# Performance work log

Measured on AMD Instinct MI355X. Metric: run time of the kernel, lower is better.

Reference implementation:

```python
import jax, jax.numpy as jnp
import numpy as np

N = 2048  # number of graph nodes


def setup_inputs() -> dict:
    key = jax.random.key(0)
    k1, k2, k3, k4 = jax.random.split(key, 4)
    # dense non-negative adjacency / association matrix
    A = jax.random.uniform(k1, (N, N), dtype=jnp.float32)
    # GTConv weights: layer0.conv1, layer0.conv2, layer1.conv1 (each (2,1,1,1))
    w1a = jax.random.normal(k2, (2, 1, 1, 1), dtype=jnp.float32)
    w1b = jax.random.normal(k3, (2, 1, 1, 1), dtype=jnp.float32)
    w2a = jax.random.normal(k4, (2, 1, 1, 1), dtype=jnp.float32)
    return {"A": A, "w1a": w1a, "w1b": w1b, "w2a": w2a}


def _gtconv(A4, w):
    # A4: (1,1,n,n); w: (2,1,1,1). softmax over dim=1 (singleton -> ones),
    # broadcast-multiply -> (2,1,n,n), sum over dim 0 -> (1,n,n)
    sw = jax.nn.softmax(w, axis=1)
    return jnp.sum(A4 * sw, axis=0)


def _norm(H):
    # H: (n,n). H <- diag(deg)^-1 @ (H + I), expressed as a row-scale
    # (identical math to the diagonal mm in the original).
    n = H.shape[0]
    H = H + jnp.eye(n, dtype=H.dtype)
    deg = jnp.sum(H, axis=1)
    deg = jnp.where(deg <= 1e-10, jnp.ones_like(deg), deg)
    return H / deg[:, None]


def reference(A, w1a, w1b, w2a):
    A4 = A[None, None]  # (1,1,n,n) after the forward's unsqueeze + broadcast
    # layer 0 (first=True)
    a = _gtconv(A4, w1a)            # (1,n,n)
    b = _gtconv(A4, w1b)            # (1,n,n)
    H = jnp.matmul(a, b)            # (1,n,n)
    # layer 1 (first=False): normalization of H[0], then bmm with conv(A)
    H_ = _norm(H[0])[None]          # (1,n,n)
    a2 = _gtconv(A4, w2a)           # (1,n,n)
    H2 = jnp.matmul(H_, a2)         # (1,n,n)
    return H2
```

## Files before the change

kernel.cpp:

```cpp
#include <hip/hip_runtime.h>
#include <stdint.h>

#define N 2048
#define TILE 128
#define BK 32
#define KI (N / BK)
#define LDSW 40
#define NN ((size_t)N * (size_t)N)

typedef unsigned short u16;
typedef __bf16 bf16x8 __attribute__((ext_vector_type(8)));
typedef unsigned short ushortx8 __attribute__((ext_vector_type(8)));
typedef float floatx4 __attribute__((ext_vector_type(4)));

static __device__ __forceinline__ u16 f2bf(float f) {
  unsigned int u = __builtin_bit_cast(unsigned int, f);
  return (u16)((u + 0x7fffu + ((u >> 16) & 1u)) >> 16);
}
static __device__ __forceinline__ float bf2f(u16 h) {
  unsigned int u = ((unsigned int)h) << 16;
  return __builtin_bit_cast(float, u);
}

__global__ void cast_tr(const float* __restrict__ A, u16* __restrict__ Ab,
                        u16* __restrict__ Abt) {
  __shared__ float tile[32][33];
  const int tx = threadIdx.x, ty = threadIdx.y;
  const int c = blockIdx.x * 32 + tx;
#pragma unroll
  for (int i = 0; i < 4; i++) {
    const int r = blockIdx.y * 32 + ty + i * 8;
    const float v = A[r * N + c];
    Ab[r * N + c] = f2bf(v);
    tile[ty + i * 8][tx] = v;
  }
  __syncthreads();
  const int r2 = blockIdx.y * 32 + tx;
#pragma unroll
  for (int i = 0; i < 4; i++) {
    const int c2 = blockIdx.x * 32 + ty + i * 8;
    Abt[c2 * N + r2] = f2bf(tile[tx][ty + i * 8]);
  }
}

__device__ __forceinline__ void gemm_core(const u16* __restrict__ L,
                                          const u16* __restrict__ Rt,
                                          floatx4 acc[4][2]) {
  __shared__ __align__(16) u16 As[2][TILE * LDSW];
  __shared__ __align__(16) u16 Bs[2][TILE * LDSW];

  const int t = threadIdx.x;
  const int row0 = blockIdx.y * TILE;
  const int col0 = blockIdx.x * TILE;

  const int srow = t >> 2;
  const int sc = (t & 3) * 8;
  const u16* gA = L + (size_t)(row0 + srow) * N + sc;
  const u16* gB = Rt + (size_t)(col0 + srow) * N + sc;
  const int woff = srow * LDSW + sc;

  const int lane = t & 63;
  const int w = t >> 6;
  const int wr = (w >> 2) * 64;
  const int wc = (w & 3) * 32;
  const int lr = lane & 15;
  const int q = lane >> 4;
  const int aoff = (wr + lr) * LDSW + q * 8;
  const int boff = (wc + lr) * LDSW + q * 8;

#pragma unroll
  for (int i = 0; i < 4; i++)
#pragma unroll
    for (int j = 0; j < 2; j++) acc[i][j] = (floatx4){0.f, 0.f, 0.f, 0.f};

  ushortx8 rA[4], rB[4];
#pragma unroll
  for (int s = 0; s < 3; s++) {
    rA[s] = *(const ushortx8*)(gA + s * BK);
    rB[s] = *(const ushortx8*)(gB + s * BK);
  }
  *(ushortx8*)(&As[0][woff]) = rA[0];
  *(ushortx8*)(&Bs[0][woff]) = rB[0];
  __syncthreads();

#define GSTEP(i, s, cur, nxt)                                                \
  {                                                                          \
    if ((i) + 3 < KI) {                                                      \
      rA[((s) + 3) & 3] = *(const ushortx8*)(gA + ((i) + 3) * BK);           \
      rB[((s) + 3) & 3] = *(const ushortx8*)(gB + ((i) + 3) * BK);           \
    }                                                                        \
    bf16x8 af[4], bfr[2];                                                    \
    _Pragma("unroll") for (int mt = 0; mt < 4; mt++) af[mt] =                \
        __builtin_bit_cast(bf16x8,                                           \
                           *(const ushortx8*)&As[cur][aoff + mt * 16 * LDSW]); \
    _Pragma("unroll") for (int nt = 0; nt < 2; nt++) bfr[nt] =               \
        __builtin_bit_cast(bf16x8,                                           \
                           *(const ushortx8*)&Bs[cur][boff + nt * 16 * LDSW]); \
    _Pragma("unroll") for (int mt = 0; mt < 4; mt++)                         \
        _Pragma("unroll") for (int nt = 0; nt < 2; nt++) acc[mt][nt] =       \
            __builtin_amdgcn_mfma_f32_16x16x32_bf16(af[mt], bfr[nt],         \
                                                    acc[mt][nt], 0, 0, 0);   \
    __syncthreads();   \
    if ((i) + 1 < KI) {                                                      \
      *(ushortx8*)(&As[nxt][woff]) = rA[((s) + 1) & 3];                      \
      *(ushortx8*)(&Bs[nxt][woff]) = rB[((s) + 1) & 3];                      \
    }                                                                        \
    __syncthreads();                      \
  }

  for (int io = 0; io < KI; io += 4) {
    GSTEP(io + 0, 0, 0, 1)
    GSTEP(io + 1, 1, 1, 0)
    GSTEP(io + 2, 2, 0, 1)
    GSTEP(io + 3, 3, 1, 0)
  }
#undef GSTEP
}

__global__ __launch_bounds__(512, 2) void gemm_aa(const u16* __restrict__ Ab,
                                                  const u16* __restrict__ Abt,
                                                  u16* __restrict__ Mb) {
  floatx4 acc[4][2];
  gemm_core(Ab, Abt, acc);
  const int t = threadIdx.x;
  const int lane = t & 63, w = t >> 6;
  const int wr = (w >> 2) * 64, wc = (w & 3) * 32;
  const int lr = lane & 15, q = lane >> 4;
  const int row0 = blockIdx.y * TILE, col0 = blockIdx.x * TILE;
#pragma unroll
  for (int mt = 0; mt < 4; mt++)
#pragma unroll
    for (int r = 0; r < 4; r++) {
      const int rr = row0 + wr + mt * 16 + q * 4 + r;
#pragma unroll
      for (int nt = 0; nt < 2; nt++) {
        const int cc = col0 + wc + nt * 16 + lr;
        Mb[(size_t)rr * N + cc] = f2bf(acc[mt][nt][r]);
      }
    }
}

__global__ void rowsum_k(const u16* __restrict__ Mb, float* __restrict__ rdeg) {
  const int row = blockIdx.x;
  const int t = threadIdx.x;
  const ushortx8 v = *((const ushortx8*)(Mb + (size_t)row * N) + t);
  float s = 0.f;
#pragma unroll
  for (int j = 0; j < 8; j++) s += bf2f(v[j]);
#pragma unroll
  for (int off = 32; off > 0; off >>= 1) s += __shfl_down(s, off, 64);
  __shared__ float ws[4];
  if ((t & 63) == 0) ws[t >> 6] = s;
  __syncthreads();
  if (t == 0) {
    float d = 4.f * (ws[0] + ws[1] + ws[2] + ws[3]) + 1.f;
    if (d <= 1e-10f) d = 1.f;
    rdeg[row] = 1.f / d;
  }
}

__global__ __launch_bounds__(512, 2) void gemm_ma(const u16* __restrict__ Mb,
                                                  const u16* __restrict__ Abt,
                                                  const float* __restrict__ A,
                                                  const float* __restrict__ rdeg,
                                                  float* __restrict__ out) {
  floatx4 acc[4][2];
  gemm_core(Mb, Abt, acc);
  const int t = threadIdx.x;
  const int lane = t & 63, w = t >> 6;
  const int wr = (w >> 2) * 64, wc = (w & 3) * 32;
  const int lr = lane & 15, q = lane >> 4;
  const int row0 = blockIdx.y * TILE, col0 = blockIdx.x * TILE;
#pragma unroll
  for (int mt = 0; mt < 4; mt++)
#pragma unroll
    for (int r = 0; r < 4; r++) {
      const int rr = row0 + wr + mt * 16 + q * 4 + r;
      const float rd = rdeg[rr];
#pragma unroll
      for (int nt = 0; nt < 2; nt++) {
        const int cc = col0 + wc + nt * 16 + lr;
        out[(size_t)rr * N + cc] =
            (8.f * acc[mt][nt][r] + 2.f * A[(size_t)rr * N + cc]) * rd;
      }
    }
}

extern "C" void kernel_launch(void* const* d_in, const int* in_sizes, int n_in,
                              void* d_out, int out_size, void* d_ws, size_t ws_size,
                              hipStream_t stream) {
  const float* A = (const float*)d_in[0];
  float* out = (float*)d_out;
  char* ws = (char*)d_ws;
  u16* Ab = (u16*)ws;
  u16* Abt = (u16*)(ws + NN * 2);
  u16* Mb = (u16*)(ws + NN * 4);
  float* rdeg = (float*)(ws + NN * 6);

  cast_tr<<<dim3(N / 32, N / 32), dim3(32, 8), 0, stream>>>(A, Ab, Abt);
  gemm_aa<<<dim3(N / TILE, N / TILE), 512, 0, stream>>>(Ab, Abt, Mb);
  rowsum_k<<<N, 256, 0, stream>>>(Mb, rdeg);
  gemm_ma<<<dim3(N / TILE, N / TILE), 512, 0, stream>>>(Mb, Abt, A, rdeg, out);
}
```

Measured before the change: 138.4 us.

## Double the GEMM K-tile and use a single barrier per pipelined step

Raises the K tile from 32 to 64 (LDS row pitch 72) so each thread stages two 8-element vectors per row, and each step issues two MFMA sub-iterations. The register prefetch ring goes from four slots to two. The pipeline now writes the next LDS buffer straight after compute and syncs once per step instead of twice. Together these halve the barriers per K element and amortise loop overhead. In exchange LDS use and register pressure rise, which could limit two-block occupancy. Index math in the cast kernel is also widened to size_t.

```diff
diff --git a/kernel.cpp b/kernel.cpp
--- a/kernel.cpp
+++ b/kernel.cpp
@@ -3,9 +3,9 @@
 
 #define N 2048
 #define TILE 128
-#define BK 32
+#define BK 64
 #define KI (N / BK)
-#define LDSW 40
+#define LDSW 72
 #define NN ((size_t)N * (size_t)N)
 
 typedef unsigned short u16;
@@ -30,8 +30,8 @@
 #pragma unroll
   for (int i = 0; i < 4; i++) {
     const int r = blockIdx.y * 32 + ty + i * 8;
-    const float v = A[r * N + c];
-    Ab[r * N + c] = f2bf(v);
+    const float v = A[(size_t)r * N + c];
+    Ab[(size_t)r * N + c] = f2bf(v);
     tile[ty + i * 8][tx] = v;
   }
   __syncthreads();
@@ -39,7 +39,7 @@
 #pragma unroll
   for (int i = 0; i < 4; i++) {
     const int c2 = blockIdx.x * 32 + ty + i * 8;
-    Abt[c2 * N + r2] = f2bf(tile[tx][ty + i * 8]);
+    Abt[(size_t)c2 * N + r2] = f2bf(tile[tx][ty + i * 8]);
   }
 }
 
@@ -54,7 +54,7 @@
   const int col0 = blockIdx.x * TILE;
 
   const int srow = t >> 2;
-  const int sc = (t & 3) * 8;
+  const int sc = (t & 3) * 16;
   const u16* gA = L + (size_t)(row0 + srow) * N + sc;
   const u16* gB = Rt + (size_t)(col0 + srow) * N + sc;
   const int woff = srow * LDSW + sc;
@@ -65,54 +65,62 @@
   const int wc = (w & 3) * 32;
   const int lr = lane & 15;
   const int q = lane >> 4;
-  const int aoff = (wr + lr) * LDSW + q * 8;
-  const int boff = (wc + lr) * LDSW + q * 8;
+  const int abase = (wr + lr) * LDSW + q * 8;
+  const int bbase = (wc + lr) * LDSW + q * 8;
 
 #pragma unroll
   for (int i = 0; i < 4; i++)
 #pragma unroll
     for (int j = 0; j < 2; j++) acc[i][j] = (floatx4){0.f, 0.f, 0.f, 0.f};
 
-  ushortx8 rA[4], rB[4];
-#pragma unroll
-  for (int s = 0; s < 3; s++) {
-    rA[s] = *(const ushortx8*)(gA + s * BK);
-    rB[s] = *(const ushortx8*)(gB + s * BK);
-  }
-  *(ushortx8*)(&As[0][woff]) = rA[0];
-  *(ushortx8*)(&Bs[0][woff]) = rB[0];
+  ushortx8 sA[2][2], sB[2][2];
+  sA[0][0] = *(const ushortx8*)(gA);
+  sA[0][1] = *(const ushortx8*)(gA + 8);
+  sB[0][0] = *(const ushortx8*)(gB);
+  sB[0][1] = *(const ushortx8*)(gB + 8);
+  sA[1][0] = *(const ushortx8*)(gA + BK);
+  sA[1][1] = *(const ushortx8*)(gA + BK + 8);
+  sB[1][0] = *(const ushortx8*)(gB + BK);
+  sB[1][1] = *(const ushortx8*)(gB + BK + 8);
+  *(ushortx8*)&As[0][woff] = sA[0][0];
+  *(ushortx8*)&As[0][woff + 8] = sA[0][1];
+  *(ushortx8*)&Bs[0][woff] = sB[0][0];
+  *(ushortx8*)&Bs[0][woff + 8] = sB[0][1];
   __syncthreads();
 
-#define GSTEP(i, s, cur, nxt)                                                \
-  {                                                                          \
-    if ((i) + 3 < KI) {                                                      \
-      rA[((s) + 3) & 3] = *(const ushortx8*)(gA + ((i) + 3) * BK);           \
-      rB[((s) + 3) & 3] = *(const ushortx8*)(gB + ((i) + 3) * BK);           \
-    }                                                                        \
-    bf16x8 af[4], bfr[2];                                                    \
-    _Pragma("unroll") for (int mt = 0; mt < 4; mt++) af[mt] =                \
-        __builtin_bit_cast(bf16x8,                                           \
-                           *(const ushortx8*)&As[cur][aoff + mt * 16 * LDSW]); \
-    _Pragma("unroll") for (int nt = 0; nt < 2; nt++) bfr[nt] =               \
-        __builtin_bit_cast(bf16x8,                                           \
-                           *(const ushortx8*)&Bs[cur][boff + nt * 16 * LDSW]); \
-    _Pragma("unroll") for (int mt = 0; mt < 4; mt++)                         \
-        _Pragma("unroll") for (int nt = 0; nt < 2; nt++) acc[mt][nt] =       \
-            __builtin_amdgcn_mfma_f32_16x16x32_bf16(af[mt], bfr[nt],         \
-                                                    acc[mt][nt], 0, 0, 0);   \
-    __syncthreads();   \
-    if ((i) + 1 < KI) {                                                      \
-      *(ushortx8*)(&As[nxt][woff]) = rA[((s) + 1) & 3];                      \
-      *(ushortx8*)(&Bs[nxt][woff]) = rB[((s) + 1) & 3];                      \
-    }                                                                        \
-    __syncthreads();                      \
-  }
-
-  for (int io = 0; io < KI; io += 4) {
-    GSTEP(io + 0, 0, 0, 1)
-    GSTEP(io + 1, 1, 1, 0)
-    GSTEP(io + 2, 2, 0, 1)
-    GSTEP(io + 3, 3, 1, 0)
+#define GSTEP(i, cur, nxt)                                                    \
+  {                                                                           \
+    if ((i) + 2 < KI) {                                                       \
+      sA[cur][0] = *(const ushortx8*)(gA + ((i) + 2) * BK);                   \
+      sA[cur][1] = *(const ushortx8*)(gA + ((i) + 2) * BK + 8);               \
+      sB[cur][0] = *(const ushortx8*)(gB + ((i) + 2) * BK);                   \
+      sB[cur][1] = *(const ushortx8*)(gB + ((i) + 2) * BK + 8);               \
+    }                                                                         \
+    _Pragma("unroll") for (int kk = 0; kk < 2; kk++) {                        \
+      bf16x8 af[4], bfr[2];                                                   \
+      _Pragma("unroll") for (int mt = 0; mt < 4; mt++) af[mt] =               \
+          __builtin_bit_cast(bf16x8,                                          \
+              *(const ushortx8*)&As[cur][abase + kk * 32 + mt * 16 * LDSW]);  \
+      _Pragma("unroll") for (int nt = 0; nt < 2; nt++) bfr[nt] =              \
+          __builtin_bit_cast(bf16x8,                                          \
+              *(const ushortx8*)&Bs[cur][bbase + kk * 32 + nt * 16 * LDSW]);  \
+      _Pragma("unroll") for (int mt = 0; mt < 4; mt++)                        \
+          _Pragma("unroll") for (int nt = 0; nt < 2; nt++) acc[mt][nt] =      \
+              __builtin_amdgcn_mfma_f32_16x16x32_bf16(af[mt], bfr[nt],        \
+                                                      acc[mt][nt], 0, 0, 0);  \
+    }                                                                         \
+    if ((i) + 1 < KI) {                                                       \
+      *(ushortx8*)&As[nxt][woff] = sA[nxt][0];                                \
+      *(ushortx8*)&As[nxt][woff + 8] = sA[nxt][1];                            \
+      *(ushortx8*)&Bs[nxt][woff] = sB[nxt][0];                                \
+      *(ushortx8*)&Bs[nxt][woff + 8] = sB[nxt][1];                            \
+    }                                                                         \
+    __syncthreads();                                                          \
+  }
+
+  for (int io = 0; io < KI; io += 2) {
+    GSTEP(io, 0, 1)
+    GSTEP(io + 1, 1, 0)
   }
 #undef GSTEP
 }
```

Result: faster. 134.9 us (-2.5%).
